# Optimization experiments

Measured on AMD Instinct MI355X. Metric: run time of the kernel, lower is better.

Reference implementation:

```python
import jax, jax.numpy as jnp
import numpy as np

B, N, DIM = 4, 4096, 768
H = 12
DH = DIM // H          # 64
S = 16                 # num_segments
M = N // S             # 256 segment_len
SCALE = DH ** -0.5


def setup_inputs() -> dict:
    key = jax.random.key(0)
    ks = jax.random.split(key, 7)
    std = DIM ** -0.5
    return {
        "x": jax.random.normal(ks[0], (B, N, DIM), dtype=jnp.float32),
        "Wq": jax.random.normal(ks[1], (DIM, DIM), dtype=jnp.float32) * std,
        "Wkv": jax.random.normal(ks[2], (DIM, DIM), dtype=jnp.float32) * std,
        "Wo": jax.random.normal(ks[3], (DIM, DIM), dtype=jnp.float32) * std,
        "bo": jax.random.normal(ks[4], (DIM,), dtype=jnp.float32) * 0.02,
        "Wo0": jax.random.normal(ks[5], (DIM, DIM), dtype=jnp.float32) * std,
        "bo0": jax.random.normal(ks[6], (DIM,), dtype=jnp.float32) * 0.02,
    }


def _rotary_freqs(n, dh, dtype):
    # lucidrains RotaryEmbedding: inv_freq over even dims, emb = cat(freqs, freqs)
    inv_freq = 1.0 / (10000.0 ** (jnp.arange(0, dh, 2, dtype=jnp.float32) / dh))
    t = jnp.arange(n, dtype=jnp.float32)
    freqs = jnp.einsum("n,f->nf", t, inv_freq)           # (n, dh/2)
    return jnp.concatenate([freqs, freqs], axis=-1).astype(dtype)  # (n, dh)


def _rotate_half(t):
    # '... (j d) -> ... j d', j=2 ; (-x2, x1)
    x1, x2 = jnp.split(t, 2, axis=-1)
    return jnp.concatenate([-x2, x1], axis=-1)


def _apply_rotary(freqs, t):
    # freqs: (1, n, dh) broadcast over (bh, n, dh); rot_dim == dh here
    return t * jnp.cos(freqs) + _rotate_half(t) * jnp.sin(freqs)


def reference(x, Wq, Wkv, Wo, bo, Wo0, bo0):
    b, n, dim = x.shape
    q = x @ Wq            # (b, n, dim), bias-free
    kv = x @ Wkv          # shared K==V projection

    def to_heads(t):      # 'b n (h d) -> (b h) n d'
        return t.reshape(b, n, H, DH).transpose(0, 2, 1, 3).reshape(b * H, n, DH)

    q, kv = to_heads(q), to_heads(kv)

    freqs = _rotary_freqs(n, DH, x.dtype)[None, :, :]    # (1, n, dh)
    q = _apply_rotary(freqs, q)
    kv = _apply_rotary(freqs, kv)

    q = q * SCALE
    c = b * H
    qs = q.reshape(c, S, M, DH)
    kvs = kv.reshape(c, S, M, DH)

    # adjacent-segment KV windows: segment t attends to [t-1, t] for t>=1
    kvs_ccs = jnp.concatenate([kvs[:, :-1], kvs[:, 1:]], axis=2)  # (c, S-1, 2M, dh)
    qs_ccs = qs[:, 1:]                                            # (c, S-1, M, dh)

    lsim = jnp.einsum("csmd,csnd->csmn", qs_ccs, kvs_ccs)         # (c, S-1, M, 2M)
    attn1 = jax.nn.softmax(lsim, axis=-1)
    out1 = jnp.einsum("csmn,csnd->csmd", attn1, kvs_ccs)          # (c, S-1, M, dh)

    # global (self) attention within first segment
    q0, kv0 = qs[:, 0], kvs[:, 0]                                 # (c, M, dh)
    sim0 = jnp.einsum("cmd,cnd->cmn", q0, kv0)
    attn0 = jax.nn.softmax(sim0, axis=-1)
    out0 = jnp.einsum("cmn,cnd->cmd", attn0, kv0)                 # (c, M, dh)

    def merge_heads(t, nn):  # '(b h) nn d -> b nn (h d)'
        return t.reshape(b, H, nn, DH).transpose(0, 2, 1, 3).reshape(b, nn, H * DH)

    out_1 = merge_heads(out1.reshape(c, (S - 1) * M, DH), (S - 1) * M)
    out_0 = merge_heads(out0, M)

    out_1o = out_1 @ Wo + bo
    out_0o = out_0 @ Wo0 + bo0
    return jnp.concatenate([out_0o, out_1o], axis=1)              # (b, n, dim)
```

## Files before the change

### kernel.cpp

```cpp
#include <hip/hip_runtime.h>
#include <hip/hip_bf16.h>


typedef float f32x4 __attribute__((ext_vector_type(4)));
typedef short bf16x8 __attribute__((ext_vector_type(8)));

#define DEV static __device__ __forceinline__

DEV short f2bf(float f) {
  union { __hip_bfloat16 h; unsigned short u; } cv;
  cv.h = __float2bfloat16(f);
  return (short)cv.u;
}

DEV f32x4 fz4() { f32x4 z = {0.f, 0.f, 0.f, 0.f}; return z; }

DEV void gload16(const void* g, void* l) {
  __builtin_amdgcn_global_load_lds((const __attribute__((address_space(1))) void*)g,
                                   (__attribute__((address_space(3))) void*)l, 16, 0, 0);
}

__global__ void __launch_bounds__(256) k_rope(float* __restrict__ cosT,
                                              float* __restrict__ sinT) {
  int idx = blockIdx.x * 256 + threadIdx.x;
  int pos = idx >> 5, jm = idx & 31;
  float invf = exp2f(-(float)jm * (13.287712379549449f / 32.0f));
  float th = (float)pos * invf;
  cosT[idx] = cosf(th);
  sinT[idx] = sinf(th);
}

__global__ void __launch_bounds__(256) k_cvtx(const float* __restrict__ x,
                                              short* __restrict__ xb) {
  int i = (blockIdx.x * 256 + threadIdx.x) * 8;
  float4 a = *(const float4*)(x + i);
  float4 b = *(const float4*)(x + i + 4);
  bf16x8 v;
  v[0] = f2bf(a.x); v[1] = f2bf(a.y); v[2] = f2bf(a.z); v[3] = f2bf(a.w);
  v[4] = f2bf(b.x); v[5] = f2bf(b.y); v[6] = f2bf(b.z); v[7] = f2bf(b.w);
  *(bf16x8*)(xb + i) = v;
}

__global__ void __launch_bounds__(256) k_transw(const float* __restrict__ Wq,
                                                const float* __restrict__ Wkv,
                                                const float* __restrict__ Wo,
                                                const float* __restrict__ Wo0,
                                                short* __restrict__ WtQKV,
                                                short* __restrict__ WtO) {
  __shared__ float t[64][65];
  int z = blockIdx.z;
  const float* src = (z == 0) ? Wq : (z == 1) ? Wkv : (z == 2) ? Wo : Wo0;
  short* dst = (z < 2) ? (WtQKV + (size_t)z * (768 * 768))
                       : (WtO + (size_t)(z - 2) * (768 * 768));
  int k0 = blockIdx.x * 64, j0 = blockIdx.y * 64;
  int tc = threadIdx.x & 63, tr = threadIdx.x >> 6;
#pragma unroll
  for (int i = 0; i < 16; i++) {
    int r = i * 4 + tr;
    t[tc][r] = src[(size_t)(k0 + r) * 768 + j0 + tc];
  }
  __syncthreads();
#pragma unroll
  for (int i = 0; i < 16; i++) {
    int r = i * 4 + tr;
    dst[(size_t)(j0 + r) * 768 + k0 + tc] = f2bf(t[r][tc]);
  }
}

#define QSTAGE(Abuf, Bbuf, Abase, Bbase, kt)                                   \
  {                                                                            \
    _Pragma("unroll") for (int i = 0; i < 2; i++) {                            \
      int rowi = i * 64 + wid * 16 + (lane >> 2);                              \
      int cci = (kt) * 64 + ((((lane & 3) ^ (rowi & 3)) << 4));                \
      gload16((Abase) + (size_t)(r0 + rowi) * 1536 + cci,                      \
              (char*)(Abuf) + i * 4096 + wid * 1024);                          \
      gload16((Bbase) + (size_t)(j0 + rowi) * 1536 + cci,                      \
              (char*)(Bbuf) + i * 4096 + wid * 1024);                          \
    }                                                                          \
  }

__global__ void __launch_bounds__(256, 4) k_gemm_qkv(
    const short* __restrict__ xb, const short* __restrict__ Wt,
    const float* __restrict__ cosT, const float* __restrict__ sinT,
    short* __restrict__ Qb, short* __restrict__ KVb) {
  __shared__ short Al[2][4096];
  __shared__ short Bl[2][4096];
  int r0 = blockIdx.x * 128;
  int cbk = blockIdx.y;
  bool isQ = cbk < 6;
  int cbl = isQ ? cbk : cbk - 6;
  const char* Ab = (const char*)xb;
  const char* Bb = (const char*)(Wt + (isQ ? (size_t)0 : (size_t)(768 * 768)));
  int j0 = cbl * 128;
  int tid = threadIdx.x, lane = tid & 63, wid = tid >> 6;
  int wr = wid >> 1, wc = wid & 1;
  int l15 = lane & 15, lg = lane >> 4;
  int rsw = (l15 & 3) << 4;

  f32x4 acc[4][4];
#pragma unroll
  for (int i = 0; i < 4; i++)
#pragma unroll
    for (int j = 0; j < 4; j++) acc[i][j] = fz4();

  QSTAGE(Al[0], Bl[0], Ab, Bb, 0)
  for (int kt = 0; kt < 24; kt++) {
    int cb = kt & 1;
    __syncthreads();
    if (kt + 1 < 24) QSTAGE(Al[cb ^ 1], Bl[cb ^ 1], Ab, Bb, kt + 1)
    const char* Ac = (const char*)Al[cb];
    const char* Bc = (const char*)Bl[cb];
    bf16x8 af[4], bfr[4];
#pragma unroll
    for (int mr = 0; mr < 4; mr++)
      af[mr] = *(const bf16x8*)(Ac + (wr * 64 + mr * 16 + l15) * 64 + ((lg * 16) ^ rsw));
#pragma unroll
    for (int nc = 0; nc < 4; nc++)
      bfr[nc] = *(const bf16x8*)(Bc + (wc * 64 + nc * 16 + l15) * 64 + ((lg * 16) ^ rsw));
#pragma unroll
    for (int mr = 0; mr < 4; mr++)
#pragma unroll
      for (int nc = 0; nc < 4; nc++)
        acc[mr][nc] = __builtin_amdgcn_mfma_f32_16x16x32_bf16(af[mr], bfr[nc], acc[mr][nc], 0, 0, 0);
  }

  int h = 2 * cbl + wc;
  short* Ob = isQ ? Qb : KVb;
  float scl = isQ ? 0.18033688011112042f : 1.0f;
#pragma unroll
  for (int mr = 0; mr < 4; mr++) {
#pragma unroll
    for (int rg = 0; rg < 4; rg++) {
      int r = r0 + wr * 64 + mr * 16 + lg * 4 + rg;
      int b = r >> 12, pos = r & 4095;
      const float* cT = cosT + pos * 32;
      const float* sT = sinT + pos * 32;
      float c0 = cT[l15], s0 = sT[l15];
      float c1 = cT[16 + l15], s1 = sT[16 + l15];
      float v0 = acc[mr][0][rg], v1 = acc[mr][1][rg];
      float v2 = acc[mr][2][rg], v3 = acc[mr][3][rg];
      size_t base = ((size_t)((b * 12 + h) * 4096 + pos)) * 64 + l15;
      Ob[base]      = f2bf((v0 * c0 - v2 * s0) * scl);
      Ob[base + 16] = f2bf((v1 * c1 - v3 * s1) * scl);
      Ob[base + 32] = f2bf((v2 * c0 + v0 * s0) * scl);
      Ob[base + 48] = f2bf((v3 * c1 + v1 * s1) * scl);
    }
  }
}

__global__ void __launch_bounds__(256) k_transkv(const short* __restrict__ KVb,
                                                 short* __restrict__ KVt) {
  __shared__ short T[64][72];
  int c = blockIdx.x;
  int pt = blockIdx.y;
  int t = threadIdx.x;
  int ch = t & 7, rr = t >> 3;
#pragma unroll
  for (int i = 0; i < 2; i++) {
    int p = rr + i * 32;
    bf16x8 v = *(const bf16x8*)&KVb[((size_t)c * 4096 + pt * 64 + p) * 64 + ch * 8];
    *(bf16x8*)&T[p][ch * 8] = v;
  }
  __syncthreads();
#pragma unroll
  for (int i = 0; i < 2; i++) {
    int d = rr + i * 32;
    bf16x8 v;
#pragma unroll
    for (int j = 0; j < 8; j++) {
      int cc = ch * 8 + j;
      int g = cc >> 5, sig = cc & 31;
      int p = g * 32 + 4 * (sig >> 3) + (sig & 3) + 16 * ((sig >> 2) & 1);
      v[j] = T[p][d];
    }
    *(bf16x8*)&KVt[((size_t)c * 64 + d) * 4096 + pt * 64 + ch * 8] = v;
  }
}

#define STAGE(buf, kk0)                                                        \
  {                                                                            \
    _Pragma("unroll") for (int i = 0; i < 2; i++) {                            \
      gload16(KVc + (size_t)((kk0) + i * 32 + krow) * 128 + ksrccol,           \
              (char*)Kl[buf] + i * 4096 + wid * 1024);                         \
      gload16(KVtc + ((size_t)(i * 32 + krow) * 4096 + (kk0)) * 2 + ksrccol,   \
              (char*)Vl[buf] + i * 4096 + wid * 1024);                         \
    }                                                                          \
  }

__global__ void __launch_bounds__(256, 4) k_attn(const short* __restrict__ Qb,
                                                 const short* __restrict__ KVbp,
                                                 const short* __restrict__ KVtp,
                                                 short* __restrict__ AO) {
  __shared__ short Kl[2][4096];
  __shared__ short Vl[2][4096];
  int bid = blockIdx.x;
  int orig = (bid & 7) * 192 + (bid >> 3);
  int c = orig >> 5;
  int e = orig & 31;
  int s = (e < 2) ? 0 : ((e - 2) >> 1) + 1;
  int qh = (e < 2) ? e : (e - 2) & 1;
  int NC = (s == 0) ? 4 : 8;
  int Kbase = (s == 0) ? 0 : (s - 1) * 256;

  int tid = threadIdx.x, lane = tid & 63, wid = tid >> 6;
  int l15 = lane & 15, lg = lane >> 4;
  const char* KVc = (const char*)(KVbp + (size_t)c * 4096 * 64);
  const char* KVtc = (const char*)(KVtp + (size_t)c * 64 * 4096);

  int krow = tid >> 3;
  int ksrccol = ((tid & 7) * 16) ^ ((krow & 7) << 4);
  int swz = (l15 & 7) << 4;

  int q0 = s * 256 + qh * 128 + wid * 32;
  bf16x8 qf[2][2];
#pragma unroll
  for (int qt = 0; qt < 2; qt++) {
    const short* Qr = Qb + ((size_t)c * 4096 + q0 + qt * 16 + l15) * 64 + lg * 8;
    qf[qt][0] = *(const bf16x8*)Qr;
    qf[qt][1] = *(const bf16x8*)(Qr + 32);
  }

  const f32x4 mi = {-32.f, -32.f, -32.f, -32.f};
  bf16x8 ones;
#pragma unroll
  for (int j = 0; j < 8; j++) ones[j] = (short)0x3F80;

  f32x4 oacc[2][4];
  f32x4 lacc[2];
#pragma unroll
  for (int qt = 0; qt < 2; qt++) {
    lacc[qt] = fz4();
#pragma unroll
    for (int vt = 0; vt < 4; vt++) oacc[qt][vt] = fz4();
  }

  STAGE(0, Kbase)
  for (int ch = 0; ch < NC; ch++) {
    int cb = ch & 1;
    __syncthreads();
    if (ch + 1 < NC) STAGE(cb ^ 1, Kbase + (ch + 1) * 64)
    const char* Kb_ = (const char*)Kl[cb];
    const char* Vb_ = (const char*)Vl[cb];
#pragma unroll
    for (int u = 0; u < 2; u++) {
      f32x4 z[2][2];
#pragma unroll
      for (int t2 = 0; t2 < 2; t2++) {
        const char* Kp = Kb_ + ((2 * u + t2) * 16 + l15) * 128;
        bf16x8 kf0 = *(const bf16x8*)(Kp + ((lg * 16) ^ swz));
        bf16x8 kf1 = *(const bf16x8*)(Kp + ((64 + lg * 16) ^ swz));
        __builtin_amdgcn_s_setprio(1);
#pragma unroll
        for (int qt = 0; qt < 2; qt++) {
          f32x4 zz = __builtin_amdgcn_mfma_f32_16x16x32_bf16(kf0, qf[qt][0], mi, 0, 0, 0);
          zz = __builtin_amdgcn_mfma_f32_16x16x32_bf16(kf1, qf[qt][1], zz, 0, 0, 0);
          z[qt][t2] = zz;
        }
        __builtin_amdgcn_s_setprio(0);
      }
      bf16x8 pf[2];
#pragma unroll
      for (int qt = 0; qt < 2; qt++) {
#pragma unroll
        for (int t2 = 0; t2 < 2; t2++)
#pragma unroll
          for (int r = 0; r < 4; r++)
            pf[qt][t2 * 4 + r] = f2bf(exp2f(z[qt][t2][r]));
      }
      bf16x8 vf[4];
#pragma unroll
      for (int vt = 0; vt < 4; vt++)
        vf[vt] = *(const bf16x8*)(Vb_ + (vt * 16 + l15) * 128 +
                                  ((u * 64 + lg * 16) ^ swz));
      __builtin_amdgcn_s_setprio(1);
#pragma unroll
      for (int qt = 0; qt < 2; qt++) {
#pragma unroll
        for (int vt = 0; vt < 4; vt++)
          oacc[qt][vt] = __builtin_amdgcn_mfma_f32_16x16x32_bf16(pf[qt], vf[vt], oacc[qt][vt], 0, 0, 0);
        lacc[qt] = __builtin_amdgcn_mfma_f32_16x16x32_bf16(pf[qt], ones, lacc[qt], 0, 0, 0);
      }
      __builtin_amdgcn_s_setprio(0);
    }
  }

  int bq = c / 12, hh = c % 12;
#pragma unroll
  for (int qt = 0; qt < 2; qt++) {
    float rinv[4];
#pragma unroll
    for (int r = 0; r < 4; r++) rinv[r] = 1.0f / lacc[qt][r];
#pragma unroll
    for (int vt = 0; vt < 4; vt++)
#pragma unroll
      for (int r = 0; r < 4; r++) {
        size_t row = (size_t)bq * 4096 + q0 + qt * 16 + lg * 4 + r;
        AO[row * 768 + hh * 64 + vt * 16 + l15] = f2bf(oacc[qt][vt][r] * rinv[r]);
      }
  }
}

__global__ void __launch_bounds__(256, 4) k_gemm_out(
    const short* __restrict__ AO, const short* __restrict__ Wt,
    const float* __restrict__ bo, const float* __restrict__ bo0,
    float* __restrict__ out) {
  __shared__ short Al[2][4096];
  __shared__ short Bl[2][4096];
  int r0 = blockIdx.x * 128;
  int j0 = blockIdx.y * 128;
  bool o0sel = (r0 & 4095) < 256;
  const char* Ab = (const char*)AO;
  const char* Bb = (const char*)(Wt + (o0sel ? (size_t)1 : (size_t)0) * (768 * 768));
  const float* bias = o0sel ? bo0 : bo;
  int tid = threadIdx.x, lane = tid & 63, wid = tid >> 6;
  int wr = wid >> 1, wc = wid & 1;
  int l15 = lane & 15, lg = lane >> 4;
  int rsw = (l15 & 3) << 4;

  f32x4 acc[4][4];
#pragma unroll
  for (int i = 0; i < 4; i++)
#pragma unroll
    for (int j = 0; j < 4; j++) acc[i][j] = fz4();

  QSTAGE(Al[0], Bl[0], Ab, Bb, 0)
  for (int kt = 0; kt < 24; kt++) {
    int cb = kt & 1;
    __syncthreads();
    if (kt + 1 < 24) QSTAGE(Al[cb ^ 1], Bl[cb ^ 1], Ab, Bb, kt + 1)
    const char* Ac = (const char*)Al[cb];
    const char* Bc = (const char*)Bl[cb];
    bf16x8 af[4], bfr[4];
#pragma unroll
    for (int mr = 0; mr < 4; mr++)
      af[mr] = *(const bf16x8*)(Ac + (wr * 64 + mr * 16 + l15) * 64 + ((lg * 16) ^ rsw));
#pragma unroll
    for (int nc = 0; nc < 4; nc++)
      bfr[nc] = *(const bf16x8*)(Bc + (wc * 64 + nc * 16 + l15) * 64 + ((lg * 16) ^ rsw));
#pragma unroll
    for (int mr = 0; mr < 4; mr++)
#pragma unroll
      for (int nc = 0; nc < 4; nc++)
        acc[mr][nc] = __builtin_amdgcn_mfma_f32_16x16x32_bf16(af[mr], bfr[nc], acc[mr][nc], 0, 0, 0);
  }

  float bs[4];
#pragma unroll
  for (int nc = 0; nc < 4; nc++) bs[nc] = bias[j0 + wc * 64 + nc * 16 + l15];
#pragma unroll
  for (int mr = 0; mr < 4; mr++)
#pragma unroll
    for (int rg = 0; rg < 4; rg++) {
      size_t r = (size_t)r0 + wr * 64 + mr * 16 + lg * 4 + rg;
      float* op = out + r * 768 + j0 + wc * 64 + l15;
      op[0]  = acc[mr][0][rg] + bs[0];
      op[16] = acc[mr][1][rg] + bs[1];
      op[32] = acc[mr][2][rg] + bs[2];
      op[48] = acc[mr][3][rg] + bs[3];
    }
}

extern "C" void kernel_launch(void* const* d_in, const int* in_sizes, int n_in,
                              void* d_out, int out_size, void* d_ws, size_t ws_size,
                              hipStream_t stream) {
  (void)in_sizes; (void)n_in; (void)out_size; (void)ws_size;
  const float* x   = (const float*)d_in[0];
  const float* Wq  = (const float*)d_in[1];
  const float* Wkv = (const float*)d_in[2];
  const float* Wo  = (const float*)d_in[3];
  const float* bo  = (const float*)d_in[4];
  const float* Wo0 = (const float*)d_in[5];
  const float* bo0 = (const float*)d_in[6];
  float* out = (float*)d_out;

  char* ws = (char*)d_ws;
  short* xb    = (short*)(ws + 0);
  short* AO    = xb;
  short* Qb    = (short*)(ws + 25165824);
  short* KVb   = (short*)(ws + 50331648);
  short* KVt   = (short*)(ws + 75497472);
  short* WtQKV = (short*)(ws + 75497472);
  float* cosT  = (float*)(ws + 77856768);
  float* sinT  = (float*)(ws + 78381056);
  short* WtO   = (short*)(ws + 100663296);

  k_rope<<<512, 256, 0, stream>>>(cosT, sinT);
  k_cvtx<<<6144, 256, 0, stream>>>(x, xb);
  k_transw<<<dim3(12, 12, 4), 256, 0, stream>>>(Wq, Wkv, Wo, Wo0, WtQKV, WtO);
  k_gemm_qkv<<<dim3(128, 12), 256, 0, stream>>>(xb, WtQKV, cosT, sinT, Qb, KVb);
  k_transkv<<<dim3(48, 64), 256, 0, stream>>>(KVb, KVt);
  k_attn<<<1536, 256, 0, stream>>>(Qb, KVb, KVt, AO);
  k_gemm_out<<<dim3(128, 6), 256, 0, stream>>>(AO, WtO, bo, bo0, out);
}
```

Before: 155.2 us.

## Use XCD-aware block mapping for GEMMs and 512-thread attention blocks per segment

Both GEMMs now use a 1D grid whose block index is remapped so that blocks sharing the same row panel land on the same XCD, aiming to improve L2 reuse of the A operand. The attention kernel changes from 256-thread blocks covering half a segment to 512-thread blocks covering a whole 256-query segment. Each block then loads every K/V tile once for all 8 waves, and the staging code is reshaped so each thread issues one load per tile. Larger blocks raise LDS sharing but may reduce the number of resident blocks, and the launch bound was changed to (512, 6).

```diff
diff --git a/kernel.cpp b/kernel.cpp
--- a/kernel.cpp
+++ b/kernel.cpp
@@ -85,8 +85,10 @@
     short* __restrict__ Qb, short* __restrict__ KVb) {
   __shared__ short Al[2][4096];
   __shared__ short Bl[2][4096];
-  int r0 = blockIdx.x * 128;
-  int cbk = blockIdx.y;
+  int bid = blockIdx.x;
+  int xcd = bid & 7, loc = bid >> 3;
+  int r0 = (xcd * 16 + loc / 12) * 128;
+  int cbk = loc % 12;
   bool isQ = cbk < 6;
   int cbl = isQ ? cbk : cbk - 6;
   const char* Ab = (const char*)xb;
@@ -179,26 +181,22 @@
 
 #define STAGE(buf, kk0)                                                        \
   {                                                                            \
-    _Pragma("unroll") for (int i = 0; i < 2; i++) {                            \
-      gload16(KVc + (size_t)((kk0) + i * 32 + krow) * 128 + ksrccol,           \
-              (char*)Kl[buf] + i * 4096 + wid * 1024);                         \
-      gload16(KVtc + ((size_t)(i * 32 + krow) * 4096 + (kk0)) * 2 + ksrccol,   \
-              (char*)Vl[buf] + i * 4096 + wid * 1024);                         \
-    }                                                                          \
-  }
-
-__global__ void __launch_bounds__(256, 4) k_attn(const short* __restrict__ Qb,
+    gload16(KVc + (size_t)((kk0) + krow) * 128 + ksrccol,                      \
+            (char*)Kl[buf] + wid * 1024);                                      \
+    gload16(KVtc + ((size_t)krow * 4096 + (kk0)) * 2 + ksrccol,                \
+            (char*)Vl[buf] + wid * 1024);                                      \
+  }
+
+__global__ void __launch_bounds__(512, 6) k_attn(const short* __restrict__ Qb,
                                                  const short* __restrict__ KVbp,
                                                  const short* __restrict__ KVtp,
                                                  short* __restrict__ AO) {
   __shared__ short Kl[2][4096];
   __shared__ short Vl[2][4096];
   int bid = blockIdx.x;
-  int orig = (bid & 7) * 192 + (bid >> 3);
-  int c = orig >> 5;
-  int e = orig & 31;
-  int s = (e < 2) ? 0 : ((e - 2) >> 1) + 1;
-  int qh = (e < 2) ? e : (e - 2) & 1;
+  int xcd = bid & 7, loc = bid >> 3;
+  int c = xcd * 6 + loc / 16;
+  int s = loc % 16;
   int NC = (s == 0) ? 4 : 8;
   int Kbase = (s == 0) ? 0 : (s - 1) * 256;
 
@@ -211,7 +209,7 @@
   int ksrccol = ((tid & 7) * 16) ^ ((krow & 7) << 4);
   int swz = (l15 & 7) << 4;
 
-  int q0 = s * 256 + qh * 128 + wid * 32;
+  int q0 = s * 256 + wid * 32;
   bf16x8 qf[2][2];
 #pragma unroll
   for (int qt = 0; qt < 2; qt++) {
@@ -306,8 +304,10 @@
     float* __restrict__ out) {
   __shared__ short Al[2][4096];
   __shared__ short Bl[2][4096];
-  int r0 = blockIdx.x * 128;
-  int j0 = blockIdx.y * 128;
+  int bid = blockIdx.x;
+  int xcd = bid & 7, loc = bid >> 3;
+  int r0 = (xcd * 16 + loc / 6) * 128;
+  int j0 = (loc % 6) * 128;
   bool o0sel = (r0 & 4095) < 256;
   const char* Ab = (const char*)AO;
   const char* Bb = (const char*)(Wt + (o0sel ? (size_t)1 : (size_t)0) * (768 * 768));
@@ -387,8 +387,8 @@
   k_rope<<<512, 256, 0, stream>>>(cosT, sinT);
   k_cvtx<<<6144, 256, 0, stream>>>(x, xb);
   k_transw<<<dim3(12, 12, 4), 256, 0, stream>>>(Wq, Wkv, Wo, Wo0, WtQKV, WtO);
-  k_gemm_qkv<<<dim3(128, 12), 256, 0, stream>>>(xb, WtQKV, cosT, sinT, Qb, KVb);
+  k_gemm_qkv<<<1536, 256, 0, stream>>>(xb, WtQKV, cosT, sinT, Qb, KVb);
   k_transkv<<<dim3(48, 64), 256, 0, stream>>>(KVb, KVt);
-  k_attn<<<1536, 256, 0, stream>>>(Qb, KVb, KVt, AO);
-  k_gemm_out<<<dim3(128, 6), 256, 0, stream>>>(AO, WtO, bo, bo0, out);
-}
+  k_attn<<<768, 512, 0, stream>>>(Qb, KVb, KVt, AO);
+  k_gemm_out<<<768, 256, 0, stream>>>(AO, WtO, bo, bo0, out);
+}
```

Result: slower. 322.8 us (+107.9%).
